# Kernel tuning notes

Hardware: AMD Instinct MI355X
Metric: run time of the kernel (lower is better)

## Reference

```python
import jax, jax.numpy as jnp
import numpy as np

D_MODEL = 128
DEPTH = 4
LN_EPS = 1e-5


def _ssm(x, Wi, A, Wo):
    # x: [B, L, D]; Wi: [3D, D]; A: [D]; Wo: [D, D]
    z = jnp.einsum('bld,ed->ble', x, Wi)          # [B, L, 3D]
    u, i, o = jnp.split(z, 3, axis=-1)
    iu = jax.nn.sigmoid(i) * jnp.tanh(u)          # gated input, [B, L, D]
    og = jax.nn.sigmoid(o)                        # output gate
    a = jnp.minimum(jnp.exp(A), 0.999)            # decay, [D]

    def step(s, c):
        s = a * s + c
        return s, s

    s0 = jnp.zeros((x.shape[0], x.shape[2]), x.dtype)
    _, S = jax.lax.scan(step, s0, jnp.swapaxes(iu, 0, 1))  # [L, B, D]
    y = og * jnp.swapaxes(S, 0, 1)                # [B, L, D]
    return jnp.einsum('bld,ed->ble', y, Wo)


def _scan_2d(x, Wi, A, Wo):
    # x: [N, D, H, W] -> four directional 1D scans, averaged
    N, D, H, W = x.shape
    xh = jnp.transpose(x, (0, 2, 3, 1))           # [N, H, W, D]
    lr = _ssm(xh.reshape(N * H, W, D), Wi, A, Wo).reshape(N, H, W, D)
    rl = _ssm(jnp.flip(xh, 2).reshape(N * H, W, D), Wi, A, Wo).reshape(N, H, W, D)
    rl = jnp.flip(rl, 2)
    xw = jnp.transpose(x, (0, 3, 2, 1))           # [N, W, H, D]
    ud = _ssm(xw.reshape(N * W, H, D), Wi, A, Wo).reshape(N, W, H, D)
    du = _ssm(jnp.flip(xw, 2).reshape(N * W, H, D), Wi, A, Wo).reshape(N, W, H, D)
    du = jnp.flip(du, 2)
    y = (lr + rl + jnp.transpose(ud, (0, 2, 1, 3)) + jnp.transpose(du, (0, 2, 1, 3))) / 4
    return jnp.transpose(y, (0, 3, 1, 2))         # [N, D, H, W]


def setup_inputs() -> dict:
    key = jax.random.key(0)
    ks = jax.random.split(key, 8)
    D = D_MODEL
    lin = 1.0 / np.sqrt(D)
    tok = jax.random.normal(ks[0], (8, 16, D, 32, 32), jnp.float32)
    s_inp = jax.random.normal(ks[1], (DEPTH, 3 * D, D), jnp.float32) * lin
    s_A = jax.random.normal(ks[2], (DEPTH, D), jnp.float32) * -0.1
    s_out = jax.random.normal(ks[3], (DEPTH, D, D), jnp.float32) * lin
    t_inp = jax.random.normal(ks[4], (DEPTH, 3 * D, D), jnp.float32) * lin
    t_A = jax.random.normal(ks[5], (DEPTH, D), jnp.float32) * -0.1
    t_out = jax.random.normal(ks[6], (DEPTH, D, D), jnp.float32) * lin
    ln_g = jnp.ones((D,), jnp.float32)
    ln_b = jnp.zeros((D,), jnp.float32)
    return {"tok": tok, "s_inp": s_inp, "s_A": s_A, "s_out": s_out,
            "t_inp": t_inp, "t_A": t_A, "t_out": t_out,
            "ln_g": ln_g, "ln_b": ln_b}


def reference(tok, s_inp, s_A, s_out, t_inp, t_A, t_out, ln_g, ln_b):
    B, T, D, h, w = tok.shape
    x = tok
    for l in range(DEPTH):
        xs = x.reshape(B * T, D, h, w)
        xs = _scan_2d(xs, s_inp[l], s_A[l], s_out[l]).reshape(B, T, D, h, w)
        xt = jnp.transpose(xs, (0, 3, 4, 1, 2)).reshape(B * h * w, T, D)
        xt = _ssm(xt, t_inp[l], t_A[l], t_out[l]).reshape(B, h, w, T, D)
        x = x + jnp.transpose(xt, (0, 3, 4, 1, 2))
    xn = jnp.transpose(x, (0, 1, 3, 4, 2))        # [B,T,h,w,D]
    mu = jnp.mean(xn, axis=-1, keepdims=True)
    var = jnp.var(xn, axis=-1, keepdims=True)
    xn = (xn - mu) / jnp.sqrt(var + LN_EPS) * ln_g + ln_b
    return jnp.transpose(xn, (0, 1, 4, 2, 3))     # [B,T,D,h,w]
```

## Files before the change

kernel.cpp:

```cpp
#include <hip/hip_runtime.h>
#include <hip/hip_bf16.h>
#include <math.h>

#define D_MODEL 128
#define HW      1024
#define DEPTH   4
#define NIMG    128
#define B_      8
#define T_      16
#define LN_EPSF 1e-5f
#define TLN     131072
#define PS      1033

typedef short  s8  __attribute__((ext_vector_type(8)));
typedef ushort us8 __attribute__((ext_vector_type(8)));
typedef ushort us4 __attribute__((ext_vector_type(4)));
typedef float  f4  __attribute__((ext_vector_type(4)));

#define MFMA __builtin_amdgcn_mfma_f32_16x16x32_bf16

__device__ __forceinline__ float sig_(float x) { return 1.0f / (1.0f + __expf(-x)); }
__device__ __forceinline__ float tanh_(float x) { return 2.0f * sig_(2.0f * x) - 1.0f; }
__device__ __forceinline__ ushort f2b(float f) {
    __hip_bfloat16 h = __float2bfloat16(f);
    return *reinterpret_cast<ushort*>(&h);
}
__device__ __forceinline__ float b2f(ushort u) {
    __hip_bfloat16 h = *reinterpret_cast<__hip_bfloat16*>(&u);
    return __bfloat162float(h);
}

__global__ __launch_bounds__(256) void wconv_kernel(
    const float* __restrict__ src, ushort* __restrict__ dst, int n)
{
    int i = blockIdx.x * 256 + threadIdx.x;
    if (i < n) dst[i] = f2b(src[i]);
}

__device__ __forceinline__ void gates_from_lds(
    const ushort (*Xs)[136], const ushort* __restrict__ Wi,
    ushort* __restrict__ iu, ushort* __restrict__ og,
    size_t nbase, int q0, int tid)
{
    const int lane = tid & 63, wv = tid >> 6, grp = lane >> 4, lrow = lane & 15;
    const int ch0 = wv * 32;

    {
        f4 aU[4][2], aI[4][2];
        #pragma unroll
        for (int mt = 0; mt < 4; ++mt)
            #pragma unroll
            for (int nt = 0; nt < 2; ++nt) { aU[mt][nt] = (f4)0.f; aI[mt][nt] = (f4)0.f; }

        #pragma unroll
        for (int kk = 0; kk < 4; ++kk) {
            const int kb = kk * 32 + grp * 8;
            s8 xa[4], wu[2], wi[2];
            #pragma unroll
            for (int mt = 0; mt < 4; ++mt)
                xa[mt] = *reinterpret_cast<const s8*>(&Xs[mt * 16 + lrow][kb]);
            #pragma unroll
            for (int nt = 0; nt < 2; ++nt) {
                const int e = ch0 + nt * 16 + lrow;
                wu[nt] = *reinterpret_cast<const s8*>(Wi + (size_t)e * D_MODEL + kb);
                wi[nt] = *reinterpret_cast<const s8*>(Wi + (size_t)(e + 128) * D_MODEL + kb);
            }
            #pragma unroll
            for (int mt = 0; mt < 4; ++mt)
                #pragma unroll
                for (int nt = 0; nt < 2; ++nt) {
                    aU[mt][nt] = MFMA(xa[mt], wu[nt], aU[mt][nt], 0, 0, 0);
                    aI[mt][nt] = MFMA(xa[mt], wi[nt], aI[mt][nt], 0, 0, 0);
                }
        }
        #pragma unroll
        for (int mt = 0; mt < 4; ++mt)
            #pragma unroll
            for (int nt = 0; nt < 2; ++nt) {
                const int e = ch0 + nt * 16 + lrow;
                const size_t off = nbase + (size_t)e * HW + q0 + mt * 16 + grp * 4;
                us4 piu;
                #pragma unroll
                for (int i = 0; i < 4; ++i)
                    piu[i] = f2b(sig_(aI[mt][nt][i]) * tanh_(aU[mt][nt][i]));
                *reinterpret_cast<us4*>(iu + off) = piu;
            }
    }
    {
        f4 aO[4][2];
        #pragma unroll
        for (int mt = 0; mt < 4; ++mt)
            #pragma unroll
            for (int nt = 0; nt < 2; ++nt) aO[mt][nt] = (f4)0.f;

        #pragma unroll
        for (int kk = 0; kk < 4; ++kk) {
            const int kb = kk * 32 + grp * 8;
            s8 xa[4], wo[2];
            #pragma unroll
            for (int mt = 0; mt < 4; ++mt)
                xa[mt] = *reinterpret_cast<const s8*>(&Xs[mt * 16 + lrow][kb]);
            #pragma unroll
            for (int nt = 0; nt < 2; ++nt)
                wo[nt] = *reinterpret_cast<const s8*>(Wi + (size_t)(ch0 + nt * 16 + lrow + 256) * D_MODEL + kb);
            #pragma unroll
            for (int mt = 0; mt < 4; ++mt)
                #pragma unroll
                for (int nt = 0; nt < 2; ++nt)
                    aO[mt][nt] = MFMA(xa[mt], wo[nt], aO[mt][nt], 0, 0, 0);
        }
        #pragma unroll
        for (int mt = 0; mt < 4; ++mt)
            #pragma unroll
            for (int nt = 0; nt < 2; ++nt) {
                const int e = ch0 + nt * 16 + lrow;
                const size_t off = nbase + (size_t)e * HW + q0 + mt * 16 + grp * 4;
                us4 pog;
                #pragma unroll
                for (int i = 0; i < 4; ++i)
                    pog[i] = f2b(sig_(aO[mt][nt][i]));
                *reinterpret_cast<us4*>(og + off) = pog;
            }
    }
}

__global__ __launch_bounds__(256, 3) void gates_f32_kernel(
    const float* __restrict__ in, const ushort* __restrict__ Wi,
    ushort* __restrict__ iu, ushort* __restrict__ og)
{
    __shared__ ushort Xs[64][136];
    const int n   = blockIdx.x >> 4;
    const int q0  = (blockIdx.x & 15) << 6;
    const int tid = threadIdx.x;
    const size_t nbase = (size_t)n * TLN;

    #pragma unroll
    for (int it = 0; it < 8; ++it) {
        const int c  = it * 256 + tid;
        const int ch = c >> 4;
        const int qo = c & 15;
        f4 v = *reinterpret_cast<const f4*>(in + nbase + (size_t)ch * HW + q0 + qo * 4);
        #pragma unroll
        for (int j = 0; j < 4; ++j) Xs[qo * 4 + j][ch] = f2b(v[j]);
    }
    __syncthreads();
    gates_from_lds(Xs, Wi, iu, og, nbase, q0, tid);
}

__global__ __launch_bounds__(256, 2) void scan2d_kernel(
    ushort* bufG , const ushort* __restrict__ og,
    const float* __restrict__ Av)
{
    __shared__ float P[8 * PS];
    __shared__ float R[8 * PS];
    const int n   = blockIdx.x >> 4;
    const int oct = blockIdx.x & 15;
    const int tid = threadIdx.x;
    const size_t base = (size_t)n * TLN + (size_t)(oct * 8) * HW;

    us8 ogv[4];
    #pragma unroll
    for (int it = 0; it < 4; ++it) {
        const int c  = it * 256 + tid;
        const int dc = c >> 7, po = c & 127;
        ogv[it] = *reinterpret_cast<const us8*>(og + base + (size_t)dc * HW + po * 8);
    }

    #pragma unroll
    for (int it = 0; it < 4; ++it) {
        const int c  = it * 256 + tid;
        const int dc = c >> 7, po = c & 127;
        us8 v = *reinterpret_cast<const us8*>(bufG + base + (size_t)dc * HW + po * 8);
        #pragma unroll
        for (int j = 0; j < 8; ++j) {
            const int p = po * 8 + j;
            P[dc * PS + (p ^ (((p >> 5) & 7) << 2))] = b2f(v[j]);
        }
    }
    __syncthreads();

    const int dc  = tid & 7;
    const int row = tid >> 3;
    const float a = fminf(__expf(Av[oct * 8 + dc]), 0.999f);

    {
        const int swb = (row * 32) ^ ((row & 7) << 2);
        float x[32], r[32];
        #pragma unroll
        for (int j = 0; j < 32; ++j) x[j] = P[dc * PS + (swb ^ j)];
        float s = 0.f;
        #pragma unroll
        for (int j = 0; j < 32; ++j) { s = fmaf(a, s, x[j]); r[j] = s; }
        s = 0.f;
        #pragma unroll
        for (int j = 31; j >= 0; --j) { s = fmaf(a, s, x[j]); r[j] += s; }
        #pragma unroll
        for (int j = 0; j < 32; ++j) R[dc * PS + (swb ^ j)] = r[j];
    }
    __syncthreads();

    {
        float x[32], t[32];
        #pragma unroll
        for (int i = 0; i < 32; ++i) {
            const int p = i * 32 + row;
            x[i] = P[dc * PS + (p ^ ((i & 7) << 2))];
        }
        float s = 0.f;
        #pragma unroll
        for (int i = 0; i < 32; ++i) { s = fmaf(a, s, x[i]); t[i] = s; }
        s = 0.f;
        #pragma unroll
        for (int i = 31; i >= 0; --i) { s = fmaf(a, s, x[i]); t[i] += s; }
        #pragma unroll
        for (int i = 0; i < 32; ++i) {
            const int idx = dc * PS + ((i * 32 + row) ^ ((i & 7) << 2));
            P[idx] = t[i] + R[idx];
        }
    }
    __syncthreads();

    #pragma unroll
    for (int it = 0; it < 4; ++it) {
        const int c  = it * 256 + tid;
        const int dc2 = c >> 7, po = c & 127;
        us8 w;
        #pragma unroll
        for (int j = 0; j < 8; ++j) {
            const int p = po * 8 + j;
            w[j] = f2b(b2f(ogv[it][j]) * P[dc2 * PS + (p ^ (((p >> 5) & 7) << 2))] * 0.25f);
        }
        *reinterpret_cast<us8*>(bufG + base + (size_t)dc2 * HW + po * 8) = w;
    }
}

__global__ __launch_bounds__(256, 3) void fusedA_kernel(
    ushort* bufA , ushort* bufB ,
    const ushort* __restrict__ WoS, const ushort* __restrict__ WiT)
{
    __shared__ ushort Gs[64][136];
    const int n   = blockIdx.x >> 4;
    const int q0  = (blockIdx.x & 15) << 6;
    const int tid = threadIdx.x;
    const int lane = tid & 63, wv = tid >> 6, grp = lane >> 4, lrow = lane & 15;
    const int ch0 = wv * 32;
    const size_t nbase = (size_t)n * TLN;

    #pragma unroll
    for (int it = 0; it < 4; ++it) {
        const int c  = it * 256 + tid;
        const int ch = c >> 3, qo = c & 7;
        us8 v = *reinterpret_cast<const us8*>(bufA + nbase + (size_t)ch * HW + q0 + qo * 8);
        #pragma unroll
        for (int j = 0; j < 8; ++j) Gs[qo * 8 + j][ch] = v[j];
    }
    __syncthreads();

    f4 c1[2][4];
    #pragma unroll
    for (int et = 0; et < 2; ++et)
        #pragma unroll
        for (int qt = 0; qt < 4; ++qt) c1[et][qt] = (f4)0.f;

    #pragma unroll
    for (int kk = 0; kk < 4; ++kk) {
        const int kb = kk * 32 + grp * 8;
        s8 wf[2], xg[4];
        #pragma unroll
        for (int et = 0; et < 2; ++et)
            wf[et] = *reinterpret_cast<const s8*>(WoS + (size_t)(ch0 + et * 16 + lrow) * D_MODEL + kb);
        #pragma unroll
        for (int qt = 0; qt < 4; ++qt)
            xg[qt] = *reinterpret_cast<const s8*>(&Gs[qt * 16 + lrow][kb]);
        #pragma unroll
        for (int et = 0; et < 2; ++et)
            #pragma unroll
            for (int qt = 0; qt < 4; ++qt)
                c1[et][qt] = MFMA(wf[et], xg[qt], c1[et][qt], 0, 0, 0);
    }
    __syncthreads();

    #pragma unroll
    for (int et = 0; et < 2; ++et)
        #pragma unroll
        for (int qt = 0; qt < 4; ++qt) {
            us4 pk;
            #pragma unroll
            for (int i = 0; i < 4; ++i) pk[i] = f2b(c1[et][qt][i]);
            *reinterpret_cast<us4*>(&Gs[qt * 16 + lrow][ch0 + et * 16 + grp * 4]) = pk;
        }
    __syncthreads();

    gates_from_lds(Gs, WiT, bufA, bufB, nbase, q0, tid);
}

__global__ __launch_bounds__(256) void tscan_kernel(
    ushort* __restrict__ buf, const float* __restrict__ Av)
{
    const int tid = blockIdx.x * 256 + threadIdx.x;
    const int qo = tid & 127;
    const int d  = (tid >> 7) & 127;
    const int b  = tid >> 14;
    const float a = fminf(__expf(Av[d]), 0.999f);
    const size_t base = (size_t)(b * T_) * TLN + (size_t)d * HW + qo * 8;
    float st[8];
    #pragma unroll
    for (int j = 0; j < 8; ++j) st[j] = 0.f;
    #pragma unroll
    for (int t = 0; t < T_; ++t) {
        ushort* p = buf + base + (size_t)t * TLN;
        us8 v = *reinterpret_cast<us8*>(p);
        us8 w;
        #pragma unroll
        for (int j = 0; j < 8; ++j) {
            st[j] = fmaf(a, st[j], b2f(v[j]));
            w[j] = f2b(st[j]);
        }
        *reinterpret_cast<us8*>(p) = w;
    }
}

template <bool RF32>
__global__ __launch_bounds__(256, 3) void fusedB_kernel(
    ushort* bufA , ushort* bufB ,
    const ushort* __restrict__ WoT, const float* __restrict__ residf,
    const ushort* __restrict__ residb, ushort* __restrict__ Xb,
    const ushort* __restrict__ WiS2)
{
    __shared__ ushort Gs[64][136];
    const int n   = blockIdx.x >> 4;
    const int q0  = (blockIdx.x & 15) << 6;
    const int tid = threadIdx.x;
    const int lane = tid & 63, wv = tid >> 6, grp = lane >> 4, lrow = lane & 15;
    const int ch0 = wv * 32;
    const size_t nbase = (size_t)n * TLN;

    #pragma unroll
    for (int it = 0; it < 4; ++it) {
        const int c  = it * 256 + tid;
        const int ch = c >> 3, qo = c & 7;
        const size_t o = nbase + (size_t)ch * HW + q0 + qo * 8;
        us8 sv = *reinterpret_cast<const us8*>(bufA + o);
        us8 ov = *reinterpret_cast<const us8*>(bufB + o);
        #pragma unroll
        for (int j = 0; j < 8; ++j) Gs[qo * 8 + j][ch] = f2b(b2f(sv[j]) * b2f(ov[j]));
    }

    f4 r[4][2];
    #pragma unroll
    for (int mt = 0; mt < 4; ++mt)
        #pragma unroll
        for (int nt = 0; nt < 2; ++nt) {
            const size_t off = nbase + (size_t)(ch0 + nt * 16 + lrow) * HW + q0 + mt * 16 + grp * 4;
            if constexpr (RF32) {
                r[mt][nt] = *reinterpret_cast<const f4*>(residf + off);
            } else {
                us4 rb = *reinterpret_cast<const us4*>(residb + off);
                #pragma unroll
                for (int i = 0; i < 4; ++i) r[mt][nt][i] = b2f(rb[i]);
            }
        }
    __syncthreads();

    f4 C[4][2];
    #pragma unroll
    for (int mt = 0; mt < 4; ++mt)
        #pragma unroll
        for (int nt = 0; nt < 2; ++nt) C[mt][nt] = (f4)0.f;

    #pragma unroll
    for (int kk = 0; kk < 4; ++kk) {
        const int kb = kk * 32 + grp * 8;
        s8 xg[4], wf[2];
        #pragma unroll
        for (int mt = 0; mt < 4; ++mt)
            xg[mt] = *reinterpret_cast<const s8*>(&Gs[mt * 16 + lrow][kb]);
        #pragma unroll
        for (int nt = 0; nt < 2; ++nt)
            wf[nt] = *reinterpret_cast<const s8*>(WoT + (size_t)(ch0 + nt * 16 + lrow) * D_MODEL + kb);
        #pragma unroll
        for (int mt = 0; mt < 4; ++mt)
            #pragma unroll
            for (int nt = 0; nt < 2; ++nt)
                C[mt][nt] = MFMA(xg[mt], wf[nt], C[mt][nt], 0, 0, 0);
    }
    __syncthreads();

    #pragma unroll
    for (int mt = 0; mt < 4; ++mt)
        #pragma unroll
        for (int nt = 0; nt < 2; ++nt) {
            const int e    = ch0 + nt * 16 + lrow;
            const int qloc = mt * 16 + grp * 4;
            const size_t off = nbase + (size_t)e * HW + q0 + qloc;
            us4 xv;
            #pragma unroll
            for (int i = 0; i < 4; ++i)
                xv[i] = f2b(C[mt][nt][i] + r[mt][nt][i]);
            *reinterpret_cast<us4*>(Xb + off) = xv;
            #pragma unroll
            for (int i = 0; i < 4; ++i) Gs[qloc + i][e] = xv[i];
        }
    __syncthreads();
    gates_from_lds(Gs, WiS2, bufA, bufB, nbase, q0, tid);
}

__global__ __launch_bounds__(256, 3) void fusedB_ln_kernel(
    const ushort* __restrict__ bufA, const ushort* __restrict__ bufB,
    const ushort* __restrict__ WoT, const ushort* __restrict__ residb,
    float* __restrict__ Xout,
    const float* __restrict__ lng, const float* __restrict__ lnb)
{
    __shared__ ushort Gs[64][136];
    const int n   = blockIdx.x >> 4;
    const int q0  = (blockIdx.x & 15) << 6;
    const int tid = threadIdx.x;
    const int lane = tid & 63, wv = tid >> 6, grp = lane >> 4, lrow = lane & 15;
    const size_t nbase = (size_t)n * TLN;

    #pragma unroll
    for (int it = 0; it < 4; ++it) {
        const int c  = it * 256 + tid;
        const int ch = c >> 3, qo = c & 7;
        const size_t o = nbase + (size_t)ch * HW + q0 + qo * 8;
        us8 sv = *reinterpret_cast<const us8*>(bufA + o);
        us8 ov = *reinterpret_cast<const us8*>(bufB + o);
        #pragma unroll
        for (int j = 0; j < 8; ++j) Gs[qo * 8 + j][ch] = f2b(b2f(sv[j]) * b2f(ov[j]));
    }

    const int qb = q0 + wv * 16 + grp * 4;
    f4 r[8];
    #pragma unroll
    for (int et = 0; et < 8; ++et) {
        us4 rb = *reinterpret_cast<const us4*>(
            residb + nbase + (size_t)(et * 16 + lrow) * HW + qb);
        #pragma unroll
        for (int i = 0; i < 4; ++i) r[et][i] = b2f(rb[i]);
    }
    __syncthreads();

    f4 C[8];
    #pragma unroll
    for (int et = 0; et < 8; ++et) C[et] = (f4)0.f;
    #pragma unroll
    for (int kk = 0; kk < 4; ++kk) {
        const int kb = kk * 32 + grp * 8;
        s8 xa = *reinterpret_cast<const s8*>(&Gs[wv * 16 + lrow][kb]);
        #pragma unroll
        for (int et = 0; et < 8; ++et) {
            s8 wf = *reinterpret_cast<const s8*>(WoT + (size_t)(et * 16 + lrow) * D_MODEL + kb);
            C[et] = MFMA(xa, wf, C[et], 0, 0, 0);
        }
    }

    float s4[4] = {0.f,0.f,0.f,0.f}, q4[4] = {0.f,0.f,0.f,0.f};
    #pragma unroll
    for (int et = 0; et < 8; ++et)
        #pragma unroll
        for (int i = 0; i < 4; ++i) {
            const float v = C[et][i] + r[et][i];
            C[et][i] = v;
            s4[i] += v; q4[i] += v * v;
        }
    #pragma unroll
    for (int m = 1; m <= 8; m <<= 1)
        #pragma unroll
        for (int i = 0; i < 4; ++i) {
            s4[i] += __shfl_xor(s4[i], m);
            q4[i] += __shfl_xor(q4[i], m);
        }
    float mean[4], rstd[4];
    #pragma unroll
    for (int i = 0; i < 4; ++i) {
        mean[i] = s4[i] * (1.f / D_MODEL);
        rstd[i] = rsqrtf(q4[i] * (1.f / D_MODEL) - mean[i] * mean[i] + LN_EPSF);
    }
    #pragma unroll
    for (int et = 0; et < 8; ++et) {
        const int e = et * 16 + lrow;
        const float ge = lng[e], be = lnb[e];
        const size_t off = nbase + (size_t)e * HW + qb;
        f4 o;
        #pragma unroll
        for (int i = 0; i < 4; ++i)
            o[i] = (C[et][i] - mean[i]) * rstd[i] * ge + be;
        *reinterpret_cast<f4*>(Xout + off) = o;
    }
}

extern "C" void kernel_launch(void* const* d_in, const int* in_sizes, int n_in,
                              void* d_out, int out_size, void* d_ws, size_t ws_size,
                              hipStream_t stream) {
    const float* tok   = (const float*)d_in[0];
    const float* s_inp = (const float*)d_in[1];
    const float* s_A   = (const float*)d_in[2];
    const float* s_out = (const float*)d_in[3];
    const float* t_inp = (const float*)d_in[4];
    const float* t_A   = (const float*)d_in[5];
    const float* t_out = (const float*)d_in[6];
    const float* ln_g  = (const float*)d_in[7];
    const float* ln_b  = (const float*)d_in[8];

    float*  Xout = (float*)d_out;
    ushort* Abuf = (ushort*)d_ws;
    ushort* Bbuf = Abuf + (size_t)16777216;
    ushort* Xbuf = Bbuf + (size_t)16777216;
    ushort* Wbf  = Xbuf + (size_t)16777216;
    ushort* sWiB = Wbf;
    ushort* sWoB = Wbf + 196608;
    ushort* tWiB = Wbf + 262144;
    ushort* tWoB = Wbf + 458752;

    const dim3 blk256(256);

    wconv_kernel<<<768, blk256, 0, stream>>>(s_inp, sWiB, 196608);
    wconv_kernel<<<256, blk256, 0, stream>>>(s_out, sWoB, 65536);
    wconv_kernel<<<768, blk256, 0, stream>>>(t_inp, tWiB, 196608);
    wconv_kernel<<<256, blk256, 0, stream>>>(t_out, tWoB, 65536);

    gates_f32_kernel<<<2048, blk256, 0, stream>>>(tok, sWiB, Abuf, Bbuf);

    for (int l = 0; l < DEPTH; ++l) {
        scan2d_kernel<<<2048, blk256, 0, stream>>>(Abuf, Bbuf, s_A + (size_t)l * 128);
        fusedA_kernel<<<2048, blk256, 0, stream>>>(
            Abuf, Bbuf, sWoB + (size_t)l * 16384, tWiB + (size_t)l * 49152);
        tscan_kernel<<<512, blk256, 0, stream>>>(Abuf, t_A + (size_t)l * 128);

        const ushort* WoT  = tWoB + (size_t)l * 16384;
        if (l == 0) {
            fusedB_kernel<true><<<2048, blk256, 0, stream>>>(
                Abuf, Bbuf, WoT, tok, nullptr, Xbuf,
                sWiB + (size_t)(l + 1) * 49152);
        } else if (l < DEPTH - 1) {
            fusedB_kernel<false><<<2048, blk256, 0, stream>>>(
                Abuf, Bbuf, WoT, nullptr, Xbuf, Xbuf,
                sWiB + (size_t)(l + 1) * 49152);
        } else {
            fusedB_ln_kernel<<<2048, blk256, 0, stream>>>(
                Abuf, Bbuf, WoT, Xbuf, Xout, ln_g, ln_b);
        }
    }
}
```

Before: 683.1 us.

## Process two 64-position tiles per fusedB block with register prefetch of next tile

Each fusedB block now handles 128 spatial positions as two 64-position tiles, halving the grid. While the first tile is being processed, the bufA/bufB loads for the second tile are issued into registers, so global load latency overlaps with compute. Launch bounds drop from 3 to 2 blocks per SIMD to leave room for the extra registers. This costs occupancy and parallelism (1024 blocks) and adds a barrier between tiles, because gates_from_lds writes bufA/bufB, which the prefetch read earlier.

```diff
diff --git a/kernel.cpp b/kernel.cpp
--- a/kernel.cpp
+++ b/kernel.cpp
@@ -321,88 +321,113 @@
 }
 
 template <bool RF32>
-__global__ __launch_bounds__(256, 3) void fusedB_kernel(
+__global__ __launch_bounds__(256, 2) void fusedB_kernel(
     ushort* bufA , ushort* bufB ,
     const ushort* __restrict__ WoT, const float* __restrict__ residf,
     const ushort* __restrict__ residb, ushort* __restrict__ Xb,
     const ushort* __restrict__ WiS2)
 {
     __shared__ ushort Gs[64][136];
-    const int n   = blockIdx.x >> 4;
-    const int q0  = (blockIdx.x & 15) << 6;
+    const int n   = blockIdx.x >> 3;
+    const int qp  = blockIdx.x & 7;
     const int tid = threadIdx.x;
     const int lane = tid & 63, wv = tid >> 6, grp = lane >> 4, lrow = lane & 15;
     const int ch0 = wv * 32;
     const size_t nbase = (size_t)n * TLN;
 
+    us8 sv[4], ov[4];
     #pragma unroll
     for (int it = 0; it < 4; ++it) {
-        const int c  = it * 256 + tid;
+        const int c = it * 256 + tid;
         const int ch = c >> 3, qo = c & 7;
-        const size_t o = nbase + (size_t)ch * HW + q0 + qo * 8;
-        us8 sv = *reinterpret_cast<const us8*>(bufA + o);
-        us8 ov = *reinterpret_cast<const us8*>(bufB + o);
-        #pragma unroll
-        for (int j = 0; j < 8; ++j) Gs[qo * 8 + j][ch] = f2b(b2f(sv[j]) * b2f(ov[j]));
-    }
-
-    f4 r[4][2];
-    #pragma unroll
-    for (int mt = 0; mt < 4; ++mt)
-        #pragma unroll
-        for (int nt = 0; nt < 2; ++nt) {
-            const size_t off = nbase + (size_t)(ch0 + nt * 16 + lrow) * HW + q0 + mt * 16 + grp * 4;
-            if constexpr (RF32) {
-                r[mt][nt] = *reinterpret_cast<const f4*>(residf + off);
-            } else {
-                us4 rb = *reinterpret_cast<const us4*>(residb + off);
-                #pragma unroll
-                for (int i = 0; i < 4; ++i) r[mt][nt][i] = b2f(rb[i]);
+        const size_t o = nbase + (size_t)ch * HW + qp * 128 + qo * 8;
+        sv[it] = *reinterpret_cast<const us8*>(bufA + o);
+        ov[it] = *reinterpret_cast<const us8*>(bufB + o);
+    }
+
+    #pragma unroll
+    for (int t = 0; t < 2; ++t) {
+        const int q0 = qp * 128 + t * 64;
+
+        #pragma unroll
+        for (int it = 0; it < 4; ++it) {
+            const int c = it * 256 + tid;
+            const int ch = c >> 3, qo = c & 7;
+            #pragma unroll
+            for (int j = 0; j < 8; ++j)
+                Gs[qo * 8 + j][ch] = f2b(b2f(sv[it][j]) * b2f(ov[it][j]));
+        }
+
+        if (t == 0) {
+            #pragma unroll
+            for (int it = 0; it < 4; ++it) {
+                const int c = it * 256 + tid;
+                const int ch = c >> 3, qo = c & 7;
+                const size_t o = nbase + (size_t)ch * HW + qp * 128 + 64 + qo * 8;
+                sv[it] = *reinterpret_cast<const us8*>(bufA + o);
+                ov[it] = *reinterpret_cast<const us8*>(bufB + o);
             }
         }
-    __syncthreads();
-
-    f4 C[4][2];
-    #pragma unroll
-    for (int mt = 0; mt < 4; ++mt)
-        #pragma unroll
-        for (int nt = 0; nt < 2; ++nt) C[mt][nt] = (f4)0.f;
-
-    #pragma unroll
-    for (int kk = 0; kk < 4; ++kk) {
-        const int kb = kk * 32 + grp * 8;
-        s8 xg[4], wf[2];
-        #pragma unroll
-        for (int mt = 0; mt < 4; ++mt)
-            xg[mt] = *reinterpret_cast<const s8*>(&Gs[mt * 16 + lrow][kb]);
-        #pragma unroll
-        for (int nt = 0; nt < 2; ++nt)
-            wf[nt] = *reinterpret_cast<const s8*>(WoT + (size_t)(ch0 + nt * 16 + lrow) * D_MODEL + kb);
-        #pragma unroll
-        for (int mt = 0; mt < 4; ++mt)
+
+        f4 r[4][2];
+        #pragma unroll
+        for (int mt = 0; mt < 4; ++mt)
+            #pragma unroll
+            for (int nt = 0; nt < 2; ++nt) {
+                const size_t off = nbase + (size_t)(ch0 + nt * 16 + lrow) * HW + q0 + mt * 16 + grp * 4;
+                if constexpr (RF32) {
+                    r[mt][nt] = *reinterpret_cast<const f4*>(residf + off);
+                } else {
+                    us4 rb = *reinterpret_cast<const us4*>(residb + off);
+                    #pragma unroll
+                    for (int i = 0; i < 4; ++i) r[mt][nt][i] = b2f(rb[i]);
+                }
+            }
+        __syncthreads();
+
+        f4 C[4][2];
+        #pragma unroll
+        for (int mt = 0; mt < 4; ++mt)
+            #pragma unroll
+            for (int nt = 0; nt < 2; ++nt) C[mt][nt] = (f4)0.f;
+
+        #pragma unroll
+        for (int kk = 0; kk < 4; ++kk) {
+            const int kb = kk * 32 + grp * 8;
+            s8 xg[4], wf[2];
+            #pragma unroll
+            for (int mt = 0; mt < 4; ++mt)
+                xg[mt] = *reinterpret_cast<const s8*>(&Gs[mt * 16 + lrow][kb]);
             #pragma unroll
             for (int nt = 0; nt < 2; ++nt)
-                C[mt][nt] = MFMA(xg[mt], wf[nt], C[mt][nt], 0, 0, 0);
-    }
-    __syncthreads();
-
-    #pragma unroll
-    for (int mt = 0; mt < 4; ++mt)
-        #pragma unroll
-        for (int nt = 0; nt < 2; ++nt) {
-            const int e    = ch0 + nt * 16 + lrow;
-            const int qloc = mt * 16 + grp * 4;
-            const size_t off = nbase + (size_t)e * HW + q0 + qloc;
-            us4 xv;
-            #pragma unroll
-            for (int i = 0; i < 4; ++i)
-                xv[i] = f2b(C[mt][nt][i] + r[mt][nt][i]);
-            *reinterpret_cast<us4*>(Xb + off) = xv;
-            #pragma unroll
-            for (int i = 0; i < 4; ++i) Gs[qloc + i][e] = xv[i];
-        }
-    __syncthreads();
-    gates_from_lds(Gs, WiS2, bufA, bufB, nbase, q0, tid);
+                wf[nt] = *reinterpret_cast<const s8*>(WoT + (size_t)(ch0 + nt * 16 + lrow) * D_MODEL + kb);
+            #pragma unroll
+            for (int mt = 0; mt < 4; ++mt)
+                #pragma unroll
+                for (int nt = 0; nt < 2; ++nt)
+                    C[mt][nt] = MFMA(xg[mt], wf[nt], C[mt][nt], 0, 0, 0);
+        }
+        __syncthreads();
+
+        #pragma unroll
+        for (int mt = 0; mt < 4; ++mt)
+            #pragma unroll
+            for (int nt = 0; nt < 2; ++nt) {
+                const int e    = ch0 + nt * 16 + lrow;
+                const int qloc = mt * 16 + grp * 4;
+                const size_t off = nbase + (size_t)e * HW + q0 + qloc;
+                us4 xv;
+                #pragma unroll
+                for (int i = 0; i < 4; ++i)
+                    xv[i] = f2b(C[mt][nt][i] + r[mt][nt][i]);
+                *reinterpret_cast<us4*>(Xb + off) = xv;
+                #pragma unroll
+                for (int i = 0; i < 4; ++i) Gs[qloc + i][e] = xv[i];
+            }
+        __syncthreads();
+        gates_from_lds(Gs, WiS2, bufA, bufB, nbase, q0, tid);
+        if (t == 0) __syncthreads();
+    }
 }
 
 __global__ __launch_bounds__(256, 3) void fusedB_ln_kernel(
@@ -529,11 +554,11 @@
 
         const ushort* WoT  = tWoB + (size_t)l * 16384;
         if (l == 0) {
-            fusedB_kernel<true><<<2048, blk256, 0, stream>>>(
+            fusedB_kernel<true><<<1024, blk256, 0, stream>>>(
                 Abuf, Bbuf, WoT, tok, nullptr, Xbuf,
                 sWiB + (size_t)(l + 1) * 49152);
         } else if (l < DEPTH - 1) {
-            fusedB_kernel<false><<<2048, blk256, 0, stream>>>(
+            fusedB_kernel<false><<<1024, blk256, 0, stream>>>(
                 Abuf, Bbuf, WoT, nullptr, Xbuf, Xbuf,
                 sWiB + (size_t)(l + 1) * 49152);
         } else {
```

New measurement: 698.2 us. 1.02x slower.
